# Kernel tuning notes

Hardware: AMD Instinct MI355X
Metric: run time of the kernel (lower is better)

Reference implementation:

```python
import jax, jax.numpy as jnp
import numpy as np

CHUNK = 1024
HEAD_DIM = 128

def setup_inputs() -> dict:
    key = jax.random.key(0)
    k1, k2, k3 = jax.random.split(key, 3)
    B, H, S, D = 2, 16, 4096, HEAD_DIM
    q = jax.random.normal(k1, (B, H, S, D), dtype=jnp.float32)
    k = jax.random.normal(k2, (B, H, S, D), dtype=jnp.float32)
    v = jax.random.normal(k3, (B, H, S, D), dtype=jnp.float32)
    return {"q": q, "k": k, "v": v}

def reference(q, k, v):
    # Faithful to the torch module INCLUDING its masking bug: for every chunk
    # the triu mask uses diagonal=1 in chunk-local coordinates, so chunk-local
    # query row i attends only keys j<=i, i.e. only the first CHUNK keys matter.
    B, H, S, D = q.shape
    scale = D ** (-0.5)
    n = S // CHUNK
    qc = q.reshape(B, H, n, CHUNK, D)           # [B,H,n,C,D]
    kc = k[:, :, :CHUNK, :]                      # [B,H,C,D]
    vc = v[:, :, :CHUNK, :]                      # [B,H,C,D]
    scores = jnp.einsum('bhnid,bhjd->bhnij', qc, kc) * scale  # [B,H,n,C,C]
    mask = jnp.triu(jnp.ones((CHUNK, CHUNK), dtype=bool), 1)   # j > i masked
    scores = jnp.where(mask, -jnp.inf, scores)
    probs = jax.nn.softmax(scores, axis=-1)
    out = jnp.einsum('bhnij,bhjd->bhnid', probs, vc)
    return out.reshape(B, H, S, D)
```

## Files before the change

kernel.cpp:

```cpp
#include <hip/hip_runtime.h>


typedef __attribute__((ext_vector_type(8))) short bfrag_t;
typedef __attribute__((ext_vector_type(16))) float f32x16;
typedef unsigned short u16;
typedef unsigned int   u32;

#define SEQ     4096
#define SCHUNK  1024
#define HD      128
#define NTILE   16
#define TILE_E  8192

__device__ __forceinline__ u16 f2bf(float f) {
    union { float f; unsigned u; } x; x.f = f;
    unsigned r = x.u + 0x7fffu + ((x.u >> 16) & 1u);
    return (u16)(r >> 16);
}

__global__ __launch_bounds__(256)
void mea_prep(const float* __restrict__ kg, const float* __restrict__ vg,
              u16* __restrict__ wsK, u16* __restrict__ wsV)
{
    const int tid  = threadIdx.x;
    const int tile = blockIdx.x;
    const int bh = tile >> 4, kt = tile & 15;
    const long gsrc = (long)bh * SEQ * HD + (long)kt * 64 * HD;
    const long gdst = (long)tile * TILE_E;

#pragma unroll
    for (int i = 0; i < 4; ++i) {
        int oid = i * 256 + tid;
        int s = oid >> 6, j = oid & 63;
        const float* kp = kg + gsrc + j * HD + s * 8;
        float4 a = *(const float4*)kp;
        float4 b = *(const float4*)(kp + 4);
        bfrag_t f;
        f[0]=f2bf(a.x); f[1]=f2bf(a.y); f[2]=f2bf(a.z); f[3]=f2bf(a.w);
        f[4]=f2bf(b.x); f[5]=f2bf(b.y); f[6]=f2bf(b.z); f[7]=f2bf(b.w);
        *(bfrag_t*)(wsK + gdst + (s * 64 + j) * 8) = f;
    }
#pragma unroll
    for (int i = 0; i < 4; ++i) {
        int oid = i * 256 + tid;
        int sv = oid >> 7, d = oid & 127;
        const float* vp = vg + gsrc + sv * 8 * HD + d;
        bfrag_t f;
#pragma unroll
        for (int jj = 0; jj < 8; ++jj) f[jj] = f2bf(vp[jj * HD]);
        *(bfrag_t*)(wsV + gdst + (sv * 128 + d) * 8) = f;
    }
}

__device__ __forceinline__ void gll16(const u16* g, u16* l) {
    __builtin_amdgcn_global_load_lds((const __attribute__((address_space(1))) u32*)g,
                                     (__attribute__((address_space(3))) u32*)l, 16, 0, 0);
}

__device__ __forceinline__ float tsum16(const f32x16& p) {
    float a0 = (p[0] + p[1]) + (p[2] + p[3]);
    float a1 = (p[4] + p[5]) + (p[6] + p[7]);
    float a2 = (p[8] + p[9]) + (p[10] + p[11]);
    float a3 = (p[12] + p[13]) + (p[14] + p[15]);
    return (a0 + a1) + (a2 + a3);
}

__device__ __forceinline__ void sm_cvt(f32x16& s, float& lsum, bfrag_t* pf) {
#pragma unroll
    for (int r = 0; r < 16; ++r) s[r] = exp2f(s[r]);
    lsum += tsum16(s);
    u32 W[8];
#pragma unroll
    for (int t2 = 0; t2 < 8; ++t2)
        asm("v_cvt_pk_bf16_f32 %0, %1, %2"
            : "=v"(W[t2]) : "v"(s[2 * t2]), "v"(s[2 * t2 + 1]));
#pragma unroll
    for (int u2 = 0; u2 < 2; ++u2) {
        u32 x0 = W[4 * u2 + 0], y0 = W[4 * u2 + 2];
        u32 x1 = W[4 * u2 + 1], y1 = W[4 * u2 + 3];
        asm("v_permlane32_swap_b32 %0, %1" : "+v"(x0), "+v"(y0));
        asm("v_permlane32_swap_b32 %0, %1" : "+v"(x1), "+v"(y1));
        union { u32 w[4]; bfrag_t f; } cvt;
        cvt.w[0] = x0; cvt.w[1] = x1; cvt.w[2] = y0; cvt.w[3] = y1;
        pf[u2] = cvt.f;
    }
}

__global__ __launch_bounds__(512, 2)
void mea_main(const float* __restrict__ qg, const u16* __restrict__ wsK,
              const u16* __restrict__ wsV, float* __restrict__ og)
{
    __shared__ __align__(16) u16 K_s[2][TILE_E];
    __shared__ __align__(16) u16 V_s[2][TILE_E];

    const int tid  = threadIdx.x;
    const int lane = tid & 63;
    const int wv   = tid >> 6;
    const int c31  = lane & 31;
    const int hi   = lane >> 5;
    const int ch   = wv & 3;
    const int h    = wv >> 2;

    const int x   = blockIdx.x & 7;
    const int idx = blockIdx.x >> 3;
    const int bh  = x * 4 + (idx & 3);
    const int p   = idx >> 2;

    const long bhrow = (long)bh * SEQ + (long)ch * SCHUNK + (long)h * 32;
    const u16* Kb = wsK + (long)bh * NTILE * TILE_E;
    const u16* Vb = wsV + (long)bh * NTILE * TILE_E;
    const int so   = wv * 1024 + lane * 8;
    const int ldsb = wv * 1024;
    const float qs = 0.12751723f;

    const int kfo = hi * 512 + c31 * 8;
    const int vfo = hi * 1024 + c31 * 8;

#pragma unroll
    for (int c = 0; c < 2; ++c) {
        gll16(Kb + so + c * 512, &K_s[0][ldsb + c * 512]);
        gll16(Vb + so + c * 512, &V_s[0][ldsb + c * 512]);
    }

    int cur = 0;
    for (int seg = 0; seg < 2; ++seg) {
        const int qt = seg ? p : (15 - p);
        const int nt = qt + 1;
        const long rowbase = bhrow + (long)qt * 64;

        bfrag_t qf[8];
        {
            const float* qp = qg + (rowbase + c31) * HD + hi * 8;
#pragma unroll
            for (int ks = 0; ks < 8; ++ks) {
                float4 a = *(const float4*)(qp + ks * 16);
                float4 b = *(const float4*)(qp + ks * 16 + 4);
                bfrag_t f;
                f[0]=f2bf(a.x*qs); f[1]=f2bf(a.y*qs); f[2]=f2bf(a.z*qs); f[3]=f2bf(a.w*qs);
                f[4]=f2bf(b.x*qs); f[5]=f2bf(b.y*qs); f[6]=f2bf(b.z*qs); f[7]=f2bf(b.w*qs);
                qf[ks] = f;
            }
        }

        f32x16 oacc[4];
#pragma unroll
        for (int d = 0; d < 4; ++d)
#pragma unroll
            for (int i = 0; i < 16; ++i) oacc[d][i] = 0.f;
        float lsum = 0.f;

        for (int kt = 0; kt < nt; ++kt) {
            __syncthreads();

            if (kt + 1 < nt) {
                const long tb = (long)(kt + 1) * TILE_E;
#pragma unroll
                for (int c = 0; c < 2; ++c) {
                    gll16(Kb + tb + so + c * 512, &K_s[cur ^ 1][ldsb + c * 512]);
                    gll16(Vb + tb + so + c * 512, &V_s[cur ^ 1][ldsb + c * 512]);
                }
            } else if (seg == 0) {
#pragma unroll
                for (int c = 0; c < 2; ++c) {
                    gll16(Kb + so + c * 512, &K_s[cur ^ 1][ldsb + c * 512]);
                    gll16(Vb + so + c * 512, &V_s[cur ^ 1][ldsb + c * 512]);
                }
            }

            const bool diag = (kt == nt - 1);
            const bool do1  = !(diag && h == 0);
            bfrag_t pfA[2], pfB[2];

            const u16* kbase = &K_s[cur][kfo];
            const u16* vbase = &V_s[cur][vfo];

            {
                f32x16 s;
#pragma unroll
                for (int i = 0; i < 16; ++i) s[i] = 0.f;
                __builtin_amdgcn_s_setprio(1);
#pragma unroll
                for (int ks = 0; ks < 8; ++ks) {
                    bfrag_t kf = *(const bfrag_t*)(kbase + ks * 1024);
                    s = __builtin_amdgcn_mfma_f32_32x32x16_bf16(kf, qf[ks], s, 0, 0, 0);
                }
                __builtin_amdgcn_s_setprio(0);
                if (diag && h == 0) {
#pragma unroll
                    for (int r = 0; r < 16; ++r) {
                        int crow = (r & 3) + 8 * (r >> 2) + 4 * hi;
                        if (crow > c31) s[r] = -1e30f;
                    }
                }
                sm_cvt(s, lsum, pfA);
            }
            if (do1) {
                f32x16 s;
#pragma unroll
                for (int i = 0; i < 16; ++i) s[i] = 0.f;
                __builtin_amdgcn_s_setprio(1);
#pragma unroll
                for (int ks = 0; ks < 8; ++ks) {
                    bfrag_t kf = *(const bfrag_t*)(kbase + ks * 1024 + 256);
                    s = __builtin_amdgcn_mfma_f32_32x32x16_bf16(kf, qf[ks], s, 0, 0, 0);
                }
                __builtin_amdgcn_s_setprio(0);
                if (diag) {
#pragma unroll
                    for (int r = 0; r < 16; ++r) {
                        int crow = (r & 3) + 8 * (r >> 2) + 4 * hi;
                        if (crow > c31) s[r] = -1e30f;
                    }
                }
                sm_cvt(s, lsum, pfB);
            }

            __builtin_amdgcn_s_setprio(1);
#pragma unroll
            for (int dg = 0; dg < 4; ++dg) {
#pragma unroll
                for (int jsl = 0; jsl < 2; ++jsl) {
                    bfrag_t vf = *(const bfrag_t*)(vbase + jsl * 2048 + dg * 256);
                    oacc[dg] = __builtin_amdgcn_mfma_f32_32x32x16_bf16(vf, pfA[jsl], oacc[dg], 0, 0, 0);
                }
                if (do1) {
#pragma unroll
                    for (int jsl = 0; jsl < 2; ++jsl) {
                        bfrag_t vf = *(const bfrag_t*)(vbase + (jsl + 2) * 2048 + dg * 256);
                        oacc[dg] = __builtin_amdgcn_mfma_f32_32x32x16_bf16(vf, pfB[jsl], oacc[dg], 0, 0, 0);
                    }
                }
            }
            __builtin_amdgcn_s_setprio(0);

            cur ^= 1;
        }

        lsum += __shfl_xor(lsum, 32);
        float inv = 1.f / lsum;
#pragma unroll
        for (int dg = 0; dg < 4; ++dg) {
#pragma unroll
            for (int rq = 0; rq < 4; ++rq) {
                float4 v;
                v.x = oacc[dg][rq * 4 + 0] * inv;
                v.y = oacc[dg][rq * 4 + 1] * inv;
                v.z = oacc[dg][rq * 4 + 2] * inv;
                v.w = oacc[dg][rq * 4 + 3] * inv;
                *(float4*)(og + (rowbase + c31) * HD + dg * 32 + rq * 8 + hi * 4) = v;
            }
        }
    }
}

extern "C" void kernel_launch(void* const* d_in, const int* in_sizes, int n_in,
                              void* d_out, int out_size, void* d_ws, size_t ws_size,
                              hipStream_t stream)
{
    (void)in_sizes; (void)n_in; (void)out_size; (void)ws_size;
    const float* q = (const float*)d_in[0];
    const float* k = (const float*)d_in[1];
    const float* v = (const float*)d_in[2];
    float* o = (float*)d_out;
    u16* wsK = (u16*)d_ws;
    u16* wsV = wsK + (size_t)32 * NTILE * TILE_E;
    mea_prep<<<dim3(512), dim3(256), 0, stream>>>(k, v, wsK, wsV);
    mea_main<<<dim3(256), dim3(512), 0, stream>>>(q, wsK, wsV, o);
}
```

Before: 75.49 us.

## Double K/V tile size to 128 keys and loop over 32-key groups

Repacks K and V into 128-key tiles and processes each tile as four 32-key groups with per-wave diagonal cutoff, halving loop iterations and block-wide barriers. This is meant to cut synchronization and prefetch overhead per key. LDS use doubles to 128KB per block, which likely prevents two blocks per CU and lowers occupancy, and causal handling becomes coarser on the last tile.

```diff
diff --git a/kernel.cpp b/kernel.cpp
--- a/kernel.cpp
+++ b/kernel.cpp
@@ -9,8 +9,8 @@
 #define SEQ     4096
 #define SCHUNK  1024
 #define HD      128
-#define NTILE   16
-#define TILE_E  8192
+#define NT2     8
+#define TILE_E2 16384
 
 __device__ __forceinline__ u16 f2bf(float f) {
     union { float f; unsigned u; } x; x.f = f;
@@ -24,24 +24,24 @@
 {
     const int tid  = threadIdx.x;
     const int tile = blockIdx.x;
-    const int bh = tile >> 4, kt = tile & 15;
-    const long gsrc = (long)bh * SEQ * HD + (long)kt * 64 * HD;
-    const long gdst = (long)tile * TILE_E;
-
-#pragma unroll
-    for (int i = 0; i < 4; ++i) {
+    const int bh = tile >> 3, kt = tile & 7;
+    const long gsrc = (long)bh * SEQ * HD + (long)kt * 128 * HD;
+    const long gdst = (long)tile * TILE_E2;
+
+#pragma unroll
+    for (int i = 0; i < 8; ++i) {
         int oid = i * 256 + tid;
-        int s = oid >> 6, j = oid & 63;
+        int s = oid >> 7, j = oid & 127;
         const float* kp = kg + gsrc + j * HD + s * 8;
         float4 a = *(const float4*)kp;
         float4 b = *(const float4*)(kp + 4);
         bfrag_t f;
         f[0]=f2bf(a.x); f[1]=f2bf(a.y); f[2]=f2bf(a.z); f[3]=f2bf(a.w);
         f[4]=f2bf(b.x); f[5]=f2bf(b.y); f[6]=f2bf(b.z); f[7]=f2bf(b.w);
-        *(bfrag_t*)(wsK + gdst + (s * 64 + j) * 8) = f;
-    }
-#pragma unroll
-    for (int i = 0; i < 4; ++i) {
+        *(bfrag_t*)(wsK + gdst + (s * 128 + j) * 8) = f;
+    }
+#pragma unroll
+    for (int i = 0; i < 8; ++i) {
         int oid = i * 256 + tid;
         int sv = oid >> 7, d = oid & 127;
         const float* vp = vg + gsrc + sv * 8 * HD + d;
@@ -90,8 +90,8 @@
 void mea_main(const float* __restrict__ qg, const u16* __restrict__ wsK,
               const u16* __restrict__ wsV, float* __restrict__ og)
 {
-    __shared__ __align__(16) u16 K_s[2][TILE_E];
-    __shared__ __align__(16) u16 V_s[2][TILE_E];
+    __shared__ __align__(16) u16 K_s[2][TILE_E2];
+    __shared__ __align__(16) u16 V_s[2][TILE_E2];
 
     const int tid  = threadIdx.x;
     const int lane = tid & 63;
@@ -107,25 +107,25 @@
     const int p   = idx >> 2;
 
     const long bhrow = (long)bh * SEQ + (long)ch * SCHUNK + (long)h * 32;
-    const u16* Kb = wsK + (long)bh * NTILE * TILE_E;
-    const u16* Vb = wsV + (long)bh * NTILE * TILE_E;
-    const int so   = wv * 1024 + lane * 8;
-    const int ldsb = wv * 1024;
+    const u16* Kb = wsK + (long)bh * NT2 * TILE_E2;
+    const u16* Vb = wsV + (long)bh * NT2 * TILE_E2;
+    const int so   = wv * 2048 + lane * 8;
+    const int ldsb = wv * 2048;
     const float qs = 0.12751723f;
 
-    const int kfo = hi * 512 + c31 * 8;
+    const int kfo = hi * 1024 + c31 * 8;
     const int vfo = hi * 1024 + c31 * 8;
 
 #pragma unroll
-    for (int c = 0; c < 2; ++c) {
+    for (int c = 0; c < 4; ++c) {
         gll16(Kb + so + c * 512, &K_s[0][ldsb + c * 512]);
         gll16(Vb + so + c * 512, &V_s[0][ldsb + c * 512]);
     }
 
     int cur = 0;
     for (int seg = 0; seg < 2; ++seg) {
-        const int qt = seg ? p : (15 - p);
-        const int nt = qt + 1;
+        const int qt  = seg ? p : (15 - p);
+        const int nt2 = (qt >> 1) + 1;
         const long rowbase = bhrow + (long)qt * 64;
 
         bfrag_t qf[8];
@@ -149,89 +149,65 @@
             for (int i = 0; i < 16; ++i) oacc[d][i] = 0.f;
         float lsum = 0.f;
 
-        for (int kt = 0; kt < nt; ++kt) {
+        for (int kt = 0; kt < nt2; ++kt) {
             __syncthreads();
 
-            if (kt + 1 < nt) {
-                const long tb = (long)(kt + 1) * TILE_E;
-#pragma unroll
-                for (int c = 0; c < 2; ++c) {
+            if (kt + 1 < nt2) {
+                const long tb = (long)(kt + 1) * TILE_E2;
+#pragma unroll
+                for (int c = 0; c < 4; ++c) {
                     gll16(Kb + tb + so + c * 512, &K_s[cur ^ 1][ldsb + c * 512]);
                     gll16(Vb + tb + so + c * 512, &V_s[cur ^ 1][ldsb + c * 512]);
                 }
             } else if (seg == 0) {
 #pragma unroll
-                for (int c = 0; c < 2; ++c) {
+                for (int c = 0; c < 4; ++c) {
                     gll16(Kb + so + c * 512, &K_s[cur ^ 1][ldsb + c * 512]);
                     gll16(Vb + so + c * 512, &V_s[cur ^ 1][ldsb + c * 512]);
                 }
             }
 
-            const bool diag = (kt == nt - 1);
-            const bool do1  = !(diag && h == 0);
-            bfrag_t pfA[2], pfB[2];
+            const bool last  = (kt == nt2 - 1);
+            const int  gdiag = last ? ((qt * 64 + h * 32 - kt * 128) >> 5) : 4;
 
             const u16* kbase = &K_s[cur][kfo];
             const u16* vbase = &V_s[cur][vfo];
 
-            {
-                f32x16 s;
-#pragma unroll
-                for (int i = 0; i < 16; ++i) s[i] = 0.f;
-                __builtin_amdgcn_s_setprio(1);
-#pragma unroll
-                for (int ks = 0; ks < 8; ++ks) {
-                    bfrag_t kf = *(const bfrag_t*)(kbase + ks * 1024);
-                    s = __builtin_amdgcn_mfma_f32_32x32x16_bf16(kf, qf[ks], s, 0, 0, 0);
+#pragma unroll
+            for (int g = 0; g < 4; ++g) {
+                if (g <= gdiag) {
+                    const bool tri = (g == gdiag);
+                    f32x16 s;
+#pragma unroll
+                    for (int i = 0; i < 16; ++i) s[i] = 0.f;
+                    __builtin_amdgcn_s_setprio(1);
+#pragma unroll
+                    for (int ks = 0; ks < 8; ++ks) {
+                        bfrag_t kf = *(const bfrag_t*)(kbase + ks * 2048 + g * 256);
+                        s = __builtin_amdgcn_mfma_f32_32x32x16_bf16(kf, qf[ks], s, 0, 0, 0);
+                    }
+                    __builtin_amdgcn_s_setprio(0);
+                    if (tri) {
+#pragma unroll
+                        for (int r = 0; r < 16; ++r) {
+                            int crow = (r & 3) + 8 * (r >> 2) + 4 * hi;
+                            if (crow > c31) s[r] = -1e30f;
+                        }
+                    }
+                    bfrag_t pf[2];
+                    sm_cvt(s, lsum, pf);
+                    __builtin_amdgcn_s_setprio(1);
+#pragma unroll
+                    for (int dg = 0; dg < 4; ++dg) {
+#pragma unroll
+                        for (int j2 = 0; j2 < 2; ++j2) {
+                            bfrag_t vf = *(const bfrag_t*)(vbase + (g * 2 + j2) * 2048 + dg * 256);
+                            oacc[dg] = __builtin_amdgcn_mfma_f32_32x32x16_bf16(vf, pf[j2], oacc[dg], 0, 0, 0);
+                        }
+                    }
+                    __builtin_amdgcn_s_setprio(0);
                 }
-                __builtin_amdgcn_s_setprio(0);
-                if (diag && h == 0) {
-#pragma unroll
-                    for (int r = 0; r < 16; ++r) {
-                        int crow = (r & 3) + 8 * (r >> 2) + 4 * hi;
-                        if (crow > c31) s[r] = -1e30f;
-                    }
-                }
-                sm_cvt(s, lsum, pfA);
-            }
-            if (do1) {
-                f32x16 s;
-#pragma unroll
-                for (int i = 0; i < 16; ++i) s[i] = 0.f;
-                __builtin_amdgcn_s_setprio(1);
-#pragma unroll
-                for (int ks = 0; ks < 8; ++ks) {
-                    bfrag_t kf = *(const bfrag_t*)(kbase + ks * 1024 + 256);
-                    s = __builtin_amdgcn_mfma_f32_32x32x16_bf16(kf, qf[ks], s, 0, 0, 0);
-                }
-                __builtin_amdgcn_s_setprio(0);
-                if (diag) {
-#pragma unroll
-                    for (int r = 0; r < 16; ++r) {
-                        int crow = (r & 3) + 8 * (r >> 2) + 4 * hi;
-                        if (crow > c31) s[r] = -1e30f;
-                    }
-                }
-                sm_cvt(s, lsum, pfB);
-            }
-
-            __builtin_amdgcn_s_setprio(1);
-#pragma unroll
-            for (int dg = 0; dg < 4; ++dg) {
-#pragma unroll
-                for (int jsl = 0; jsl < 2; ++jsl) {
-                    bfrag_t vf = *(const bfrag_t*)(vbase + jsl * 2048 + dg * 256);
-                    oacc[dg] = __builtin_amdgcn_mfma_f32_32x32x16_bf16(vf, pfA[jsl], oacc[dg], 0, 0, 0);
-                }
-                if (do1) {
-#pragma unroll
-                    for (int jsl = 0; jsl < 2; ++jsl) {
-                        bfrag_t vf = *(const bfrag_t*)(vbase + (jsl + 2) * 2048 + dg * 256);
-                        oacc[dg] = __builtin_amdgcn_mfma_f32_32x32x16_bf16(vf, pfB[jsl], oacc[dg], 0, 0, 0);
-                    }
-                }
-            }
-            __builtin_amdgcn_s_setprio(0);
+            }
 
             cur ^= 1;
         }
@@ -263,7 +239,7 @@
     const float* v = (const float*)d_in[2];
     float* o = (float*)d_out;
     u16* wsK = (u16*)d_ws;
-    u16* wsV = wsK + (size_t)32 * NTILE * TILE_E;
-    mea_prep<<<dim3(512), dim3(256), 0, stream>>>(k, v, wsK, wsV);
+    u16* wsV = wsK + (size_t)32 * NT2 * TILE_E2;
+    mea_prep<<<dim3(256), dim3(256), 0, stream>>>(k, v, wsK, wsV);
     mea_main<<<dim3(256), dim3(512), 0, stream>>>(q, wsK, wsV, o);
 }
```

Measured after the change: 68.48 us, median of 3. -9.3%, faster.
